# Optimization experiments

Hardware: AMD Instinct MI355X
Metric: run time of the kernel (lower is better)

The kernel has to match this reference:

```python
import jax, jax.numpy as jnp
import numpy as np

H_GRID = 256
W_GRID = 256


def setup_inputs() -> dict:
    key = jax.random.key(0)
    k1, k2, k3, k4 = jax.random.split(key, 4)
    B, N = 8, 32768
    in_ch, out_ch = 14, 64
    xyzp = jax.random.uniform(k1, (B, N, 4), dtype=jnp.float32)  # x,y,t,p all in [0,1]
    features = jax.random.normal(k2, (B, N, in_ch), dtype=jnp.float32)
    W = jax.random.normal(k3, (9, in_ch + 2, out_ch), dtype=jnp.float32) * 0.05  # 3x3 kernel taps
    bias = jax.random.normal(k4, (out_ch,), dtype=jnp.float32) * 0.05
    return {"xyzp": xyzp, "features": features, "W": W, "bias": bias}


def reference(xyzp, features, W, bias):
    # SparseConv: voxelize points onto an (h+1)x(w+1) grid with 'mean' pooling of
    # duplicates, run a 3x3 submanifold sparse conv (inactive sites contribute 0),
    # then map results back to point order.
    h, w = H_GRID, W_GRID
    Hd, Wd = h + 1, w + 1  # round(y*h) in [0,h]
    B, N, _ = xyzp.shape
    Cin = features.shape[-1] + 2

    # yxb coordinates (note: column order [y, x] as in _get_yxb)
    y = jnp.clip(jnp.round(xyzp[..., 1] * h), 0, h).astype(jnp.int32).reshape(-1)
    x = jnp.clip(jnp.round(xyzp[..., 0] * w), 0, w).astype(jnp.int32).reshape(-1)
    b = jnp.repeat(jnp.arange(B, dtype=jnp.int32), N)

    # per-point features: [pos, neg, features]
    p = xyzp[..., 3:4]
    f = jnp.concatenate([p, 1.0 - p, features], axis=-1).reshape(B * N, Cin)

    # InputLayer mode='mean': scatter-mean duplicate coordinates into voxels
    flat = (b * Hd + y) * Wd + x  # [B*N]
    S = B * Hd * Wd
    vox_sum = jax.ops.segment_sum(f, flat, num_segments=S)            # [S, Cin]
    cnt = jax.ops.segment_sum(jnp.ones((B * N, 1), f.dtype), flat, num_segments=S)
    vox = vox_sum / jnp.maximum(cnt, 1.0)  # inactive voxels stay exactly 0

    # Submanifold 3x3 conv evaluated at each point's (active) site.
    offs = jnp.array([(dy, dx) for dy in (-1, 0, 1) for dx in (-1, 0, 1)], jnp.int32)  # [9,2]
    ny = y[:, None] + offs[None, :, 0]  # [B*N, 9]
    nx = x[:, None] + offs[None, :, 1]
    valid = (ny >= 0) & (ny < Hd) & (nx >= 0) & (nx < Wd)
    nidx = (b[:, None] * Hd + jnp.clip(ny, 0, Hd - 1)) * Wd + jnp.clip(nx, 0, Wd - 1)
    nb = vox[nidx] * valid[..., None].astype(f.dtype)  # [B*N, 9, Cin]; inactive -> 0

    out = jnp.einsum('pkc,kcd->pd', nb, W) + bias  # [B*N, out_ch]
    return out.reshape(B, N, -1)
```

## Files before the change

kernel.cpp:

```cpp
#include <hip/hip_runtime.h>

#define HD 257
#define WD 257
#define NB (8 * HD)
#define NCHUNK 32
#define CAPC 32
#define BPTS 1024
#define COUT 64
#define LROW 17
#define GPTS 64

typedef unsigned int uint;
typedef unsigned short ushort;
typedef short short8 __attribute__((ext_vector_type(8)));
typedef float f32x4 __attribute__((ext_vector_type(4)));

__device__ __forceinline__ uint pack_bf16(float a, float b) {
    uint ua = __float_as_uint(a), ub = __float_as_uint(b);
    ua += 0x7fffu + ((ua >> 16) & 1u);
    ub += 0x7fffu + ((ub >> 16) & 1u);
    return (ua >> 16) | (ub & 0xffff0000u);
}
__device__ __forceinline__ unsigned short bf16_1(float a) {
    uint ua = __float_as_uint(a);
    ua += 0x7fffu + ((ua >> 16) & 1u);
    return (unsigned short)(ua >> 16);
}

__global__ __launch_bounds__(256) void bin_kernel(
    const float* __restrict__ xyzp,
    uint* __restrict__ cnt2,
    ushort* __restrict__ pidx,
    int N) {
    __shared__ uint hist[HD];
    const int tid = threadIdx.x;
    const int chunk = blockIdx.x;
    const int b = blockIdx.y;
    const int p0 = chunk * BPTS;
    for (int i = tid; i < HD; i += 256) hist[i] = 0u;
    __syncthreads();

    const float4* xp = reinterpret_cast<const float4*>(xyzp) + (size_t)b * N;
    uint rec[BPTS / 256];
#pragma unroll
    for (int k = 0; k < BPTS / 256; ++k) {
        int i = p0 + tid + k * 256;
        float4 v = xp[i];
        int y = (int)fminf(fmaxf(rintf(v.y * 256.0f), 0.0f), 256.0f);
        uint r = atomicAdd(&hist[y], 1u);
        rec[k] = (uint)y | (r << 9);
    }
    __syncthreads();

    for (int y = tid; y < HD; y += 256)
        cnt2[(size_t)(b * HD + y) * NCHUNK + chunk] = min(hist[y], (uint)CAPC);

#pragma unroll
    for (int k = 0; k < BPTS / 256; ++k) {
        int y = rec[k] & 511;
        uint r = rec[k] >> 9;
        if (r < CAPC)
            pidx[((size_t)(b * HD + y) * NCHUNK + chunk) * CAPC + r] =
                (ushort)(p0 + tid + k * 256);
    }
}

__global__ __launch_bounds__(256) void accum_kernel(
    const uint* __restrict__ cnt2,
    const ushort* __restrict__ pidx,
    const float* __restrict__ xyzp,
    const float* __restrict__ feat,
    uint* __restrict__ voxn,
    int logN) {
    __shared__ float l[WD * LROW];
    __shared__ uint pc[NCHUNK];
    const int tid = threadIdx.x;
    const int bucket = blockIdx.x;
    const int b = bucket / HD;
    for (int i = tid; i < WD * LROW; i += 256) l[i] = 0.0f;
    if (tid < NCHUNK)
        pc[tid] = cnt2[(size_t)bucket * NCHUNK + tid];
    __syncthreads();

#pragma unroll
    for (int s = 0; s < NCHUNK * CAPC; s += 256) {
        int slot = s + tid;
        int c = slot >> 5;
        int j = slot & (CAPC - 1);
        if ((uint)j < pc[c]) {
            uint lp = pidx[((size_t)bucket * NCHUNK + c) * CAPC + j];
            int p = (b << logN) + (int)lp;
            float4 v = reinterpret_cast<const float4*>(xyzp)[p];
            int x = (int)fminf(fmaxf(rintf(v.x * 256.0f), 0.0f), 256.0f);
            float* cell = l + x * LROW;
            atomicAdd(&cell[0], v.w);
            atomicAdd(&cell[1], 1.0f - v.w);
            const float2* f2 = reinterpret_cast<const float2*>(feat + (size_t)p * 14);
#pragma unroll
            for (int jj = 0; jj < 7; ++jj) {
                float2 fv = f2[jj];
                atomicAdd(&cell[2 + 2 * jj], fv.x);
                atomicAdd(&cell[3 + 2 * jj], fv.y);
            }
        }
    }
    __syncthreads();

    for (int x = tid; x < WD; x += 256) {
        const float* c = l + x * LROW;
        float inv = __builtin_amdgcn_rcpf(fmaxf(c[0] + c[1], 1.0f));
        uint o[8];
#pragma unroll
        for (int j = 0; j < 8; ++j)
            o[j] = pack_bf16(c[2 * j] * inv, c[2 * j + 1] * inv);
        uint4* op = reinterpret_cast<uint4*>(voxn + ((size_t)bucket * WD + x) * 8);
        op[0] = make_uint4(o[0], o[1], o[2], o[3]);
        op[1] = make_uint4(o[4], o[5], o[6], o[7]);
    }
}

__global__ __launch_bounds__(256) void gather_mfma_kernel(
    const float* __restrict__ xyzp,
    const uint* __restrict__ voxn,
    const float* __restrict__ W,
    const float* __restrict__ bias,
    float* __restrict__ out, int logN) {
    __shared__ __align__(16) char sA[GPTS * 336];
    __shared__ int sCell[GPTS];
    __shared__ uint sYX[GPTS];

    const int tid = threadIdx.x;
    const int lane = tid & 63;
    const int w = tid >> 6;
    const int p0 = blockIdx.x * GPTS;
    const int hi = lane >> 4;
    const int lo = lane & 15;

    if (tid < GPTS) {
        float4 v = reinterpret_cast<const float4*>(xyzp)[p0 + tid];
        int y = (int)fminf(fmaxf(rintf(v.y * 256.0f), 0.0f), 256.0f);
        int x = (int)fminf(fmaxf(rintf(v.x * 256.0f), 0.0f), 256.0f);
        int b = (p0 + tid) >> logN;
        sCell[tid] = (b * HD + y) * WD + x;
        sYX[tid] = ((uint)y << 16) | (uint)x;
    }

    short8 bfrag[5];
    float bv = bias[w * 16 + lo];
#pragma unroll
    for (int s = 0; s < 5; ++s) {
        int kbase = s * 32 + hi * 8;
        short8 f;
#pragma unroll
        for (int j = 0; j < 8; ++j) {
            int k = kbase + j;
            float wv = (k < 144) ? W[(size_t)k * 64 + w * 16 + lo] : 0.0f;
            f[j] = (short)bf16_1(wv);
        }
        bfrag[s] = f;
    }
    __syncthreads();

    for (int idx = tid; idx < GPTS * 18; idx += 256) {
        int i = idx / 18;
        int r = idx - i * 18;
        int seg = r / 6;
        int h = r - seg * 6;
        int kx = h >> 1;
        int half = h & 1;
        uint yx = sYX[i];
        int y = (int)(yx >> 16), x = (int)(yx & 0xffffu);
        int ny = y + seg - 1, nx = x + kx - 1;
        uint4 val = make_uint4(0, 0, 0, 0);
        if ((uint)ny <= 256u && (uint)nx <= 256u) {
            size_t ncell = (size_t)sCell[i] + (size_t)((seg - 1) * WD + (kx - 1));
            val = *reinterpret_cast<const uint4*>(
                reinterpret_cast<const char*>(voxn) + ncell * 32 + (size_t)half * 16);
        }
        *reinterpret_cast<uint4*>(sA + i * 336 + (seg * 3 + kx) * 32 + half * 16) = val;
    }
    if (tid < GPTS * 2) {
        int i = tid >> 1, h = tid & 1;
        *reinterpret_cast<uint4*>(sA + i * 336 + 288 + h * 16) = make_uint4(0, 0, 0, 0);
    }
    __syncthreads();

    f32x4 acc[4];
#pragma unroll
    for (int mt = 0; mt < 4; ++mt) acc[mt] = (f32x4){bv, bv, bv, bv};

#pragma unroll
    for (int mt = 0; mt < 4; ++mt) {
        const char* abase = sA + (mt * 16 + lo) * 336 + hi * 16;
#pragma unroll
        for (int s = 0; s < 5; ++s) {
            short8 a = *reinterpret_cast<const short8*>(abase + s * 64);
            acc[mt] = __builtin_amdgcn_mfma_f32_16x16x32_bf16(a, bfrag[s], acc[mt], 0, 0, 0);
        }
    }

#pragma unroll
    for (int mt = 0; mt < 4; ++mt)
#pragma unroll
        for (int r = 0; r < 4; ++r) {
            int row = mt * 16 + hi * 4 + r;
            out[(size_t)(p0 + row) * 64 + w * 16 + lo] = acc[mt][r];
        }
}

extern "C" void kernel_launch(void* const* d_in, const int* in_sizes, int n_in,
                              void* d_out, int out_size, void* d_ws, size_t ws_size,
                              hipStream_t stream) {
    const float* xyzp = (const float*)d_in[0];
    const float* feat = (const float*)d_in[1];
    const float* W    = (const float*)d_in[2];
    const float* bias = (const float*)d_in[3];
    float* out = (float*)d_out;

    const int BN = in_sizes[0] / 4;
    const int B = 8;
    const int N = BN / B;
    int logN = 0;
    while ((1 << logN) < N) ++logN;

    uint* cnt2 = (uint*)d_ws;
    ushort* pidx = (ushort*)((char*)cnt2 + (size_t)NB * NCHUNK * 4);
    uint* voxn = (uint*)((char*)pidx + (size_t)NB * NCHUNK * CAPC * 2);
    (void)ws_size;

    dim3 bgrid(NCHUNK, B);
    bin_kernel<<<bgrid, 256, 0, stream>>>(xyzp, cnt2, pidx, N);
    accum_kernel<<<NB, 256, 0, stream>>>(cnt2, pidx, xyzp, feat, voxn, logN);
    gather_mfma_kernel<<<BN / GPTS, 256, 0, stream>>>(xyzp, voxn, W, bias, out, logN);
}
```

Before: 67.01 us.

## Pack point features as bf16 payload into bucket slots during binning

The binning kernel now reads each point's features while it streams the input, packs p, 1-p and the 14 features into a 32-byte bf16 record plus an x coordinate, and writes them straight into the bucket slot. The accumulation kernel then reads these contiguous records instead of indirectly gathering xyzp and the features from random point positions. This is meant to turn scattered global gathers into coalesced reads and to halve the bytes moved. In exchange, the input features are rounded to bf16 before the scatter-mean, which adds precision error, and the workspace grows by a large payload buffer.

```diff
diff --git a/kernel.cpp b/kernel.cpp
--- a/kernel.cpp
+++ b/kernel.cpp
@@ -29,8 +29,10 @@
 
 __global__ __launch_bounds__(256) void bin_kernel(
     const float* __restrict__ xyzp,
+    const float* __restrict__ feat,
     uint* __restrict__ cnt2,
-    ushort* __restrict__ pidx,
+    ushort* __restrict__ xarr,
+    uint* __restrict__ payload,
     int N) {
     __shared__ uint hist[HD];
     const int tid = threadIdx.x;
@@ -41,42 +43,42 @@
     __syncthreads();
 
     const float4* xp = reinterpret_cast<const float4*>(xyzp) + (size_t)b * N;
-    uint rec[BPTS / 256];
+    const float* fb = feat + (size_t)b * N * 14;
 #pragma unroll
     for (int k = 0; k < BPTS / 256; ++k) {
         int i = p0 + tid + k * 256;
         float4 v = xp[i];
         int y = (int)fminf(fmaxf(rintf(v.y * 256.0f), 0.0f), 256.0f);
+        int x = (int)fminf(fmaxf(rintf(v.x * 256.0f), 0.0f), 256.0f);
         uint r = atomicAdd(&hist[y], 1u);
-        rec[k] = (uint)y | (r << 9);
+        if (r < CAPC) {
+            size_t base = ((size_t)(b * HD + y) * NCHUNK + chunk) * CAPC + r;
+            const float2* f2 = reinterpret_cast<const float2*>(fb + (size_t)i * 14);
+            float2 f0 = f2[0], f1 = f2[1], f2v = f2[2], f3 = f2[3];
+            float2 f4 = f2[4], f5 = f2[5], f6 = f2[6];
+            uint4* dst = reinterpret_cast<uint4*>(payload + base * 8);
+            dst[0] = make_uint4(pack_bf16(v.w, 1.0f - v.w), pack_bf16(f0.x, f0.y),
+                                pack_bf16(f1.x, f1.y), pack_bf16(f2v.x, f2v.y));
+            dst[1] = make_uint4(pack_bf16(f3.x, f3.y), pack_bf16(f4.x, f4.y),
+                                pack_bf16(f5.x, f5.y), pack_bf16(f6.x, f6.y));
+            xarr[base] = (ushort)x;
+        }
     }
     __syncthreads();
 
     for (int y = tid; y < HD; y += 256)
         cnt2[(size_t)(b * HD + y) * NCHUNK + chunk] = min(hist[y], (uint)CAPC);
-
-#pragma unroll
-    for (int k = 0; k < BPTS / 256; ++k) {
-        int y = rec[k] & 511;
-        uint r = rec[k] >> 9;
-        if (r < CAPC)
-            pidx[((size_t)(b * HD + y) * NCHUNK + chunk) * CAPC + r] =
-                (ushort)(p0 + tid + k * 256);
-    }
 }
 
 __global__ __launch_bounds__(256) void accum_kernel(
     const uint* __restrict__ cnt2,
-    const ushort* __restrict__ pidx,
-    const float* __restrict__ xyzp,
-    const float* __restrict__ feat,
-    uint* __restrict__ voxn,
-    int logN) {
+    const ushort* __restrict__ xarr,
+    const uint* __restrict__ payload,
+    uint* __restrict__ voxn) {
     __shared__ float l[WD * LROW];
     __shared__ uint pc[NCHUNK];
     const int tid = threadIdx.x;
     const int bucket = blockIdx.x;
-    const int b = bucket / HD;
     for (int i = tid; i < WD * LROW; i += 256) l[i] = 0.0f;
     if (tid < NCHUNK)
         pc[tid] = cnt2[(size_t)bucket * NCHUNK + tid];
@@ -88,19 +90,16 @@
         int c = slot >> 5;
         int j = slot & (CAPC - 1);
         if ((uint)j < pc[c]) {
-            uint lp = pidx[((size_t)bucket * NCHUNK + c) * CAPC + j];
-            int p = (b << logN) + (int)lp;
-            float4 v = reinterpret_cast<const float4*>(xyzp)[p];
-            int x = (int)fminf(fmaxf(rintf(v.x * 256.0f), 0.0f), 256.0f);
+            size_t base = ((size_t)bucket * NCHUNK + c) * CAPC + j;
+            int x = xarr[base];
+            const uint4* pp = reinterpret_cast<const uint4*>(payload + base * 8);
+            uint4 a = pp[0], bq = pp[1];
+            uint d[8] = {a.x, a.y, a.z, a.w, bq.x, bq.y, bq.z, bq.w};
             float* cell = l + x * LROW;
-            atomicAdd(&cell[0], v.w);
-            atomicAdd(&cell[1], 1.0f - v.w);
-            const float2* f2 = reinterpret_cast<const float2*>(feat + (size_t)p * 14);
-#pragma unroll
-            for (int jj = 0; jj < 7; ++jj) {
-                float2 fv = f2[jj];
-                atomicAdd(&cell[2 + 2 * jj], fv.x);
-                atomicAdd(&cell[3 + 2 * jj], fv.y);
+#pragma unroll
+            for (int jj = 0; jj < 8; ++jj) {
+                atomicAdd(&cell[2 * jj],     __uint_as_float(d[jj] << 16));
+                atomicAdd(&cell[2 * jj + 1], __uint_as_float(d[jj] & 0xffff0000u));
             }
         }
     }
@@ -224,12 +223,13 @@
     while ((1 << logN) < N) ++logN;
 
     uint* cnt2 = (uint*)d_ws;
-    ushort* pidx = (ushort*)((char*)cnt2 + (size_t)NB * NCHUNK * 4);
-    uint* voxn = (uint*)((char*)pidx + (size_t)NB * NCHUNK * CAPC * 2);
+    ushort* xarr = (ushort*)((char*)cnt2 + (size_t)NB * NCHUNK * 4);
+    uint* payload = (uint*)((char*)xarr + (size_t)NB * NCHUNK * CAPC * 2);
+    uint* voxn = (uint*)((char*)payload + (size_t)NB * NCHUNK * CAPC * 32);
     (void)ws_size;
 
     dim3 bgrid(NCHUNK, B);
-    bin_kernel<<<bgrid, 256, 0, stream>>>(xyzp, cnt2, pidx, N);
-    accum_kernel<<<NB, 256, 0, stream>>>(cnt2, pidx, xyzp, feat, voxn, logN);
+    bin_kernel<<<bgrid, 256, 0, stream>>>(xyzp, feat, cnt2, xarr, payload, N);
+    accum_kernel<<<NB, 256, 0, stream>>>(cnt2, xarr, payload, voxn);
     gather_mfma_kernel<<<BN / GPTS, 256, 0, stream>>>(xyzp, voxn, W, bias, out, logN);
 }
```

Result: slower. 69.17 us (+3.2%).

## Gather neighbor voxels directly into LDS with global_load_lds and slab layout

Applied to the files above, without the earlier changes.

The gather kernel now has each wave load its point coordinates itself and issue direct global-to-LDS loads (global_load_lds, 16 bytes per lane) for neighbor voxel halves, instead of loading into registers and storing to LDS. Out-of-bounds or padding taps point at a small zeroed buffer initialized by the bin kernel. The LDS A-tile is reorganized into 1KB slabs indexed by K-chunk so the MFMA reads match the new layout, and the intermediate sync plus index tables are removed. This relies on the zero buffer being written before the gather kernel runs and on the global_load_lds instruction being available.

```diff
diff --git a/kernel.cpp b/kernel.cpp
--- a/kernel.cpp
+++ b/kernel.cpp
@@ -14,6 +14,8 @@
 typedef unsigned short ushort;
 typedef short short8 __attribute__((ext_vector_type(8)));
 typedef float f32x4 __attribute__((ext_vector_type(4)));
+typedef __attribute__((address_space(3))) uint lds_uint;
+typedef __attribute__((address_space(1))) const uint gl_uint;
 
 __device__ __forceinline__ uint pack_bf16(float a, float b) {
     uint ua = __float_as_uint(a), ub = __float_as_uint(b);
@@ -31,12 +33,14 @@
     const float* __restrict__ xyzp,
     uint* __restrict__ cnt2,
     ushort* __restrict__ pidx,
+    uint* __restrict__ zbuf,
     int N) {
     __shared__ uint hist[HD];
     const int tid = threadIdx.x;
     const int chunk = blockIdx.x;
     const int b = blockIdx.y;
     const int p0 = chunk * BPTS;
+    if (chunk == 0 && b == 0 && tid < 4) zbuf[tid] = 0u;
     for (int i = tid; i < HD; i += 256) hist[i] = 0u;
     __syncthreads();
 
@@ -122,12 +126,11 @@
 __global__ __launch_bounds__(256) void gather_mfma_kernel(
     const float* __restrict__ xyzp,
     const uint* __restrict__ voxn,
+    const uint* __restrict__ zbuf,
     const float* __restrict__ W,
     const float* __restrict__ bias,
     float* __restrict__ out, int logN) {
-    __shared__ __align__(16) char sA[GPTS * 336];
-    __shared__ int sCell[GPTS];
-    __shared__ uint sYX[GPTS];
+    __shared__ __align__(16) char sA[20 * 1024];
 
     const int tid = threadIdx.x;
     const int lane = tid & 63;
@@ -136,13 +139,26 @@
     const int hi = lane >> 4;
     const int lo = lane & 15;
 
-    if (tid < GPTS) {
-        float4 v = reinterpret_cast<const float4*>(xyzp)[p0 + tid];
-        int y = (int)fminf(fmaxf(rintf(v.y * 256.0f), 0.0f), 256.0f);
-        int x = (int)fminf(fmaxf(rintf(v.x * 256.0f), 0.0f), 256.0f);
-        int b = (p0 + tid) >> logN;
-        sCell[tid] = (b * HD + y) * WD + x;
-        sYX[tid] = ((uint)y << 16) | (uint)x;
+    float4 v = reinterpret_cast<const float4*>(xyzp)[p0 + lane];
+    int y = (int)fminf(fmaxf(rintf(v.y * 256.0f), 0.0f), 256.0f);
+    int x = (int)fminf(fmaxf(rintf(v.x * 256.0f), 0.0f), 256.0f);
+    int b = (p0 + lane) >> logN;
+    int cell = (b * HD + y) * WD + x;
+
+#pragma unroll
+    for (int r5 = 0; r5 < 5; ++r5) {
+        int slab = r5 * 4 + w;
+        int s_ = slab >> 2, h_ = slab & 3;
+        int kn = 2 * s_ + (h_ >> 1);
+        int half = h_ & 1;
+        int seg = kn / 3, kx = kn - 3 * seg;
+        int ny = y + seg - 1, nx = x + kx - 1;
+        bool ok = (kn < 9) && ((uint)ny <= 256u) && ((uint)nx <= 256u);
+        const uint* src = ok
+            ? voxn + ((size_t)cell + (seg - 1) * WD + (kx - 1)) * 8 + half * 4
+            : zbuf;
+        __builtin_amdgcn_global_load_lds((gl_uint*)src,
+                                         (lds_uint*)(sA + slab * 1024), 16, 0, 0);
     }
 
     short8 bfrag[5];
@@ -161,40 +177,16 @@
     }
     __syncthreads();
 
-    for (int idx = tid; idx < GPTS * 18; idx += 256) {
-        int i = idx / 18;
-        int r = idx - i * 18;
-        int seg = r / 6;
-        int h = r - seg * 6;
-        int kx = h >> 1;
-        int half = h & 1;
-        uint yx = sYX[i];
-        int y = (int)(yx >> 16), x = (int)(yx & 0xffffu);
-        int ny = y + seg - 1, nx = x + kx - 1;
-        uint4 val = make_uint4(0, 0, 0, 0);
-        if ((uint)ny <= 256u && (uint)nx <= 256u) {
-            size_t ncell = (size_t)sCell[i] + (size_t)((seg - 1) * WD + (kx - 1));
-            val = *reinterpret_cast<const uint4*>(
-                reinterpret_cast<const char*>(voxn) + ncell * 32 + (size_t)half * 16);
-        }
-        *reinterpret_cast<uint4*>(sA + i * 336 + (seg * 3 + kx) * 32 + half * 16) = val;
-    }
-    if (tid < GPTS * 2) {
-        int i = tid >> 1, h = tid & 1;
-        *reinterpret_cast<uint4*>(sA + i * 336 + 288 + h * 16) = make_uint4(0, 0, 0, 0);
-    }
-    __syncthreads();
-
     f32x4 acc[4];
 #pragma unroll
     for (int mt = 0; mt < 4; ++mt) acc[mt] = (f32x4){bv, bv, bv, bv};
 
 #pragma unroll
     for (int mt = 0; mt < 4; ++mt) {
-        const char* abase = sA + (mt * 16 + lo) * 336 + hi * 16;
+        const char* abase = sA + hi * 1024 + (mt * 16 + lo) * 16;
 #pragma unroll
         for (int s = 0; s < 5; ++s) {
-            short8 a = *reinterpret_cast<const short8*>(abase + s * 64);
+            short8 a = *reinterpret_cast<const short8*>(abase + s * 4096);
             acc[mt] = __builtin_amdgcn_mfma_f32_16x16x32_bf16(a, bfrag[s], acc[mt], 0, 0, 0);
         }
     }
@@ -226,10 +218,11 @@
     uint* cnt2 = (uint*)d_ws;
     ushort* pidx = (ushort*)((char*)cnt2 + (size_t)NB * NCHUNK * 4);
     uint* voxn = (uint*)((char*)pidx + (size_t)NB * NCHUNK * CAPC * 2);
+    uint* zbuf = voxn + (size_t)(B * HD * WD) * 8;
     (void)ws_size;
 
     dim3 bgrid(NCHUNK, B);
-    bin_kernel<<<bgrid, 256, 0, stream>>>(xyzp, cnt2, pidx, N);
+    bin_kernel<<<bgrid, 256, 0, stream>>>(xyzp, cnt2, pidx, zbuf, N);
     accum_kernel<<<NB, 256, 0, stream>>>(cnt2, pidx, xyzp, feat, voxn, logN);
-    gather_mfma_kernel<<<BN / GPTS, 256, 0, stream>>>(xyzp, voxn, W, bias, out, logN);
-}
+    gather_mfma_kernel<<<BN / GPTS, 256, 0, stream>>>(xyzp, voxn, zbuf, W, bias, out, logN);
+}
```

Result: slower. 73.12 us (+9.1%).
